# Kernel tuning notes

Measured on AMD Instinct MI355X. Metric: run time of the kernel, lower is better.

Reference implementation:

```python
import jax, jax.numpy as jnp
import numpy as np
from jax import lax

N_SEEDS = 16
N_SAMPS = 32
IN_C = 3
HID = [32, 64, 64]
K = 3
H = W = 64
EPS = 1e-5


def _uniform(key, shape, bound):
    return jax.random.uniform(key, shape, jnp.float32, -bound, bound)


def setup_inputs() -> dict:
    key = jax.random.key(0)
    keys = jax.random.split(key, 32)
    inp = {"x": jax.random.normal(keys[0], (N_SEEDS, N_SAMPS, IN_C, H, W), jnp.float32)}
    c_in = IN_C
    ki = 1
    for li, c_out in enumerate(HID, start=1):
        fan_in = c_in * K * K
        # kaiming_uniform with a=sqrt(5): gain=sqrt(2/(1+5))=sqrt(1/3); bound=sqrt(3)*gain/sqrt(fan)=1/sqrt(fan)
        wb = 1.0 / np.sqrt(fan_in)
        inp[f"w{li}"] = _uniform(keys[ki], (N_SEEDS * c_out, c_in, K, K), wb); ki += 1
        inp[f"b{li}"] = _uniform(keys[ki], (N_SEEDS * c_out,), wb); ki += 1
        inp[f"g{li}"] = jnp.ones((N_SEEDS * c_out,), jnp.float32)
        inp[f"be{li}"] = jnp.zeros((N_SEEDS * c_out,), jnp.float32)
        c_in = c_out
    return inp


def _layer(h, w, b, g, be):
    # grouped conv: groups = N_SEEDS, OIHW weights, NCHW data, stride 1, pad 1
    h = lax.conv_general_dilated(
        h, w, window_strides=(1, 1), padding=((1, 1), (1, 1)),
        feature_group_count=N_SEEDS,
        dimension_numbers=("NCHW", "OIHW", "NCHW"))
    h = h + b[None, :, None, None]
    # BatchNorm2d, training mode: batch statistics over (N, H, W), biased variance
    mean = jnp.mean(h, axis=(0, 2, 3))
    var = jnp.var(h, axis=(0, 2, 3))
    h = (h - mean[None, :, None, None]) * (g / jnp.sqrt(var + EPS))[None, :, None, None] + be[None, :, None, None]
    return jax.nn.relu(h)


def reference(x, w1, b1, g1, be1, w2, b2, g2, be2, w3, b3, g3, be3):
    S, N, C, Hh, Ww = x.shape  # (n_seeds, n_samps, C, H, W)
    h = jnp.swapaxes(x, 0, 1).reshape(N, S * C, Hh, Ww)
    h = _layer(h, w1, b1, g1, be1)
    h = _layer(h, w2, b2, g2, be2)
    h = _layer(h, w3, b3, g3, be3)
    c_out = HID[-1]
    h = h.reshape(N, S, c_out, Hh, Ww)
    return jnp.swapaxes(h, 0, 1)  # (n_seeds, n_samps, C_out, H, W)
```

## Files before the change

kernel.cpp:

```cpp
#include <hip/hip_runtime.h>
#include <cstddef>
#include <cstdint>

typedef __attribute__((ext_vector_type(8))) _Float16 half8;
typedef __attribute__((ext_vector_type(4))) float f32x4;
typedef _Float16 half_t;

#define NS 16
#define NN 32

static const size_t OFF_H1P = 0;
static const size_t OFF_H2P = 138412032ull;
static const size_t OFF_ZR1 = OFF_H2P + 276824064ull;
static const size_t OFF_ZR2 = OFF_ZR1 + 67584ull;
static const size_t OFF_WT1 = OFF_ZR2 + 135168ull;
static const size_t OFF_WT2 = OFF_WT1 + 55296ull;
static const size_t OFF_WT3 = OFF_WT2 + 589824ull;
static const size_t OFF_SUMS = OFF_WT3 + 1179648ull;
static const size_t OFF_PRM = OFF_SUMS + 20480ull;
static const size_t OFF_TH  = OFF_PRM + 30720ull;

static __device__ __forceinline__ half8 sr8(half8 v, half8 t) {
    half8 r = v + t;
    half8 z = {};
#if defined(__has_builtin) && __has_builtin(__builtin_elementwise_max)
    return __builtin_elementwise_max(r, z);
#else
#pragma unroll
    for (int j = 0; j < 8; ++j) r[j] = r[j] > (_Float16)0 ? r[j] : (_Float16)0;
    return r;
#endif
}

__global__ __launch_bounds__(256) void transform1_k(
    const float* __restrict__ w1, float* __restrict__ wt1)
{
    int idx = blockIdx.x * 256 + threadIdx.x;
    if (idx >= 13824) return;
    int o = idx & 31, tap = (idx >> 5) % 9, ic = (idx / 288) % 3, s = idx / 864;
    wt1[idx] = w1[((s * 32 + o) * 3 + ic) * 9 + tap];
}

__global__ __launch_bounds__(256) void wtrans2_k(
    const float* __restrict__ w2, const float* __restrict__ a1, half_t* __restrict__ wt2)
{
    int idx = blockIdx.x * 256 + threadIdx.x;
    if (idx >= 294912) return;
    int ic = idx & 31, oc = (idx >> 5) & 63, tap = (idx >> 11) % 9, s = idx / 18432;
    wt2[idx] = (half_t)(w2[((s * 64 + oc) * 32 + ic) * 9 + tap] * a1[s * 32 + ic]);
}

__global__ __launch_bounds__(256) void wtrans3_k(
    const float* __restrict__ w3, const float* __restrict__ a2, half_t* __restrict__ wt3)
{
    int idx = blockIdx.x * 256 + threadIdx.x;
    if (idx >= 589824) return;
    int ic = idx & 63, oc = (idx >> 6) & 63, tap = (idx >> 12) % 9, s = idx / 36864;
    wt3[idx] = (half_t)(w3[((s * 64 + oc) * 64 + ic) * 9 + tap] * a2[s * 64 + ic]);
}

__global__ __launch_bounds__(256) void conv1_k(
    const float* __restrict__ x, const float* __restrict__ wt1,
    const float* __restrict__ b1, half_t* __restrict__ h1p,
    float* __restrict__ sums1)
{
    __shared__ float smem[8512];
    float* xt = smem;
    float* bounce = smem;
    float* statsl = smem + 8448;
    const int tile = blockIdx.x, s = blockIdx.y, n = blockIdx.z;
    const int tx = tile & 3, ty = tile >> 2, tid = threadIdx.x;

    for (int i = tid; i < 972; i += 256) {
        int ic = i / 324, rem = i - ic * 324;
        int py = rem / 18, px = rem - py * 18;
        int gy = ty * 16 + py - 1, gx = tx * 16 + px - 1;
        float v = 0.f;
        if ((unsigned)gy < 64u && (unsigned)gx < 64u)
            v = x[(size_t)(((s * NN + n) * 3 + ic) * 64 + gy) * 64 + gx];
        xt[i] = v;
    }
    if (tid < 64) statsl[tid] = 0.f;
    __syncthreads();

    const int px = tid & 15, py = tid >> 4;
    float acc[32];
#pragma unroll
    for (int o = 0; o < 32; ++o) acc[o] = 0.f;
#pragma unroll
    for (int ic = 0; ic < 3; ++ic)
#pragma unroll
        for (int ky = 0; ky < 3; ++ky)
#pragma unroll
            for (int kx = 0; kx < 3; ++kx) {
                float v = xt[ic * 324 + (py + ky) * 18 + px + kx];
                const float* wp = wt1 + ((s * 3 + ic) * 9 + ky * 3 + kx) * 32;
#pragma unroll
                for (int o = 0; o < 32; ++o) acc[o] = fmaf(wp[o], v, acc[o]);
            }
    const float* bp = b1 + s * 32;
#pragma unroll
    for (int o = 0; o < 32; ++o) acc[o] += bp[o];

    const int gy1 = ty * 16 + py, gxp = tx * 16 + px + 1;
    half8* dst = (half8*)(h1p + (size_t)(n * NS + s) * 135168 + (size_t)(gy1 * 66 + gxp) * 32);
#pragma unroll
    for (int k = 0; k < 4; ++k) {
        half8 v8;
#pragma unroll
        for (int j = 0; j < 8; ++j) v8[j] = (half_t)acc[k * 8 + j];
        dst[k] = v8;
    }
    __syncthreads();
#pragma unroll
    for (int o = 0; o < 32; ++o) bounce[tid * 33 + o] = acc[o];
    __syncthreads();
    {
        const int oc = tid & 31, grp = tid >> 5;
        float s1 = 0.f, s2 = 0.f;
#pragma unroll 4
        for (int j = 0; j < 32; ++j) {
            float v = bounce[(grp * 32 + j) * 33 + oc];
            s1 += v; s2 += v * v;
        }
        atomicAdd(&statsl[oc * 2], s1);
        atomicAdd(&statsl[oc * 2 + 1], s2);
    }
    __syncthreads();
    if (tid < 64)
        atomicAdd(&sums1[(s * 32 + (tid >> 1)) * 2 + (tid & 1)], statsl[tid]);
}

__global__ void bnparam_k(const float* __restrict__ sums, const float* __restrict__ g,
                          const float* __restrict__ be, float* __restrict__ a,
                          float* __restrict__ b, float* __restrict__ t,
                          half_t* __restrict__ th, int C)
{
    int ch = blockIdx.x * 256 + threadIdx.x;
    if (ch >= C) return;
    const float inv = 1.f / 131072.f;
    float mean = sums[ch * 2] * inv;
    float var = sums[ch * 2 + 1] * inv - mean * mean;
    float sc = g[ch] * rsqrtf(var + 1e-5f);
    a[ch] = sc;
    float bb = be[ch] - mean * sc;
    b[ch] = bb;
    float tt = bb / sc;
    t[ch] = tt;
    th[ch] = (half_t)tt;
}

__global__ __launch_bounds__(256) void padfill_k(
    half_t* __restrict__ img, half_t* __restrict__ zrow, const float* __restrict__ t,
    int C, int c8shift, long imgstride, int rowstride, long tot_cols, long tot)
{
    long idx = (long)blockIdx.x * 256 + threadIdx.x;
    if (idx >= tot) return;
    const int nc8m = (1 << c8shift) - 1;
    if (idx < tot_cols) {
        int c8 = (int)idx & nc8m; long r = idx >> c8shift;
        int side = (int)r & 1; r >>= 1;
        int y = (int)r & 63; r >>= 6;
        int si = (int)(r & 15); int ni = (int)(r >> 4);
        half8 q;
#pragma unroll
        for (int j = 0; j < 8; ++j) q[j] = (half_t)(-(t[si * C + c8 * 8 + j] + 1.0f));
        *(half8*)(img + (long)(ni * NS + si) * imgstride + (long)y * rowstride +
                  (side ? 65 : 0) * C + c8 * 8) = q;
    } else {
        long r2 = idx - tot_cols;
        int c8 = (int)r2 & nc8m; r2 >>= c8shift;
        int xx = (int)(r2 % 66); int si = (int)(r2 / 66);
        half8 q;
#pragma unroll
        for (int j = 0; j < 8; ++j) q[j] = (half_t)(-(t[si * C + c8 * 8 + j] + 1.0f));
        *(half8*)(zrow + ((long)(si * 66 + xx)) * C + c8 * 8) = q;
    }
}

__device__ __forceinline__ void loadB2(half8 bf[4], const half_t* wb, int tap, int l15, int g) {
#pragma unroll
    for (int nt = 0; nt < 4; ++nt)
        bf[nt] = *(const half8*)(wb + (tap * 64 + nt * 16 + l15) * 32 + g * 8);
}

__device__ __forceinline__ void comp2(f32x4 acc[4][4], const half8 bf[4], const char* smem,
                                      int tap, int wv, int l15, int g) {
    const int ky = tap / 3, kx = tap - ky * 3;
#pragma unroll
    for (int mt = 0; mt < 4; ++mt) {
        int p = (wv * 4 + mt + ky) * 18 + l15 + kx;
        half8 av = *(const half8*)(smem + p * 80 + g * 16);
#pragma unroll
        for (int nt = 0; nt < 4; ++nt)
            acc[mt][nt] = __builtin_amdgcn_mfma_f32_16x16x32_f16(av, bf[nt], acc[mt][nt], 0, 0, 0);
    }
}

__global__ __launch_bounds__(256, 3) void conv2_k(
    const half_t* __restrict__ h1p, const half_t* __restrict__ zr1,
    const half_t* __restrict__ wt2, const float* __restrict__ b2,
    const half_t* __restrict__ th1, half_t* __restrict__ h2p,
    float* __restrict__ sums2)
{
    __shared__ __align__(16) char smem[37376];
    float* statsl = (float*)(smem + 36864);
    const int tile = blockIdx.x, s = blockIdx.y, n = blockIdx.z;
    const int tx = tile & 3, ty = tile >> 2, tid = threadIdx.x;
    const int l = tid & 63, wv = tid >> 6, l15 = l & 15, g = l >> 4;
    if (tid < 128) statsl[tid] = 0.f;

    const half_t* wb = wt2 + (size_t)s * 18432;
    half8 bfa[4], bfb[4];
    loadB2(bfa, wb, 0, l15, g);

    const half_t* img = h1p + (size_t)(n * NS + s) * 135168;
    const half_t* zrow = zr1 + s * 2112;
    const int j = tid & 3;
    const half8 tshj = *(const half8*)(th1 + s * 32 + j * 8);
    for (int i = tid; i < 1296; i += 256) {
        int p = i >> 2;
        int py = p / 18, pxx = p - py * 18;
        int gy = ty * 16 + py - 1;
        const half_t* rp = ((unsigned)gy < 64u) ? (img + (size_t)gy * 2112) : zrow;
        half8 v = sr8(*(const half8*)(rp + (tx * 16 + pxx) * 32 + j * 8), tshj);
        *(half8*)(smem + p * 80 + j * 16) = v;
    }
    __syncthreads();

    f32x4 acc[4][4];
#pragma unroll
    for (int mt = 0; mt < 4; ++mt)
#pragma unroll
        for (int nt = 0; nt < 4; ++nt) acc[mt][nt] = (f32x4){0.f, 0.f, 0.f, 0.f};

#pragma unroll
    for (int tap = 0; tap < 9; ++tap) {
        if (tap & 1) {
            if (tap < 8) loadB2(bfa, wb, tap + 1, l15, g);
            comp2(acc, bfb, smem, tap, wv, l15, g);
        } else {
            if (tap < 8) loadB2(bfb, wb, tap + 1, l15, g);
            comp2(acc, bfa, smem, tap, wv, l15, g);
        }
    }

    float s1a[4], s2a[4];
#pragma unroll
    for (int nt = 0; nt < 4; ++nt) {
        float bias = b2[s * 64 + nt * 16 + l15];
        float s1 = 0.f, s2 = 0.f;
#pragma unroll
        for (int mt = 0; mt < 4; ++mt)
#pragma unroll
            for (int r = 0; r < 4; ++r) {
                float v = acc[mt][nt][r] + bias;
                acc[mt][nt][r] = v;
                s1 += v; s2 += v * v;
            }
        s1 += __shfl_xor(s1, 16); s1 += __shfl_xor(s1, 32);
        s2 += __shfl_xor(s2, 16); s2 += __shfl_xor(s2, 32);
        s1a[nt] = s1; s2a[nt] = s2;
    }
    if (l < 16) {
#pragma unroll
        for (int nt = 0; nt < 4; ++nt) {
            atomicAdd(&statsl[(nt * 16 + l15) * 2], s1a[nt]);
            atomicAdd(&statsl[(nt * 16 + l15) * 2 + 1], s2a[nt]);
        }
    }
    __syncthreads();

    half_t* obuf = (half_t*)smem;
#pragma unroll
    for (int mt = 0; mt < 4; ++mt)
#pragma unroll
        for (int nt = 0; nt < 4; ++nt)
#pragma unroll
            for (int r = 0; r < 4; ++r)
                obuf[((wv * 4 + mt) * 16 + g * 4 + r) * 72 + nt * 16 + l15] = (half_t)acc[mt][nt][r];
    __syncthreads();

    half_t* img2 = h2p + (size_t)(n * NS + s) * 270336;
    for (int i = tid; i < 2048; i += 256) {
        int p = i >> 3, cc = i & 7;
        int y = ty * 16 + (p >> 4), xp = tx * 16 + (p & 15) + 1;
        *(half8*)(img2 + (size_t)y * 4224 + xp * 64 + cc * 8) = *(const half8*)(obuf + p * 72 + cc * 8);
    }
    if (tid < 128)
        atomicAdd(&sums2[(s * 64 + (tid >> 1)) * 2 + (tid & 1)], statsl[tid]);
}

__device__ __forceinline__ void loadB3(half8 bf[4][2], const half_t* wb, int tap, int l15, int g) {
#pragma unroll
    for (int nt = 0; nt < 4; ++nt) {
        const half_t* r = wb + (tap * 64 + nt * 16 + l15) * 64 + g * 8;
        bf[nt][0] = *(const half8*)(r);
        bf[nt][1] = *(const half8*)(r + 32);
    }
}

__device__ __forceinline__ void comp3(f32x4 acc[4][4], const half8 bf[4][2], const char* smem,
                                      int tap, int wv, int l15, int g) {
    const int ky = tap / 3, kx = tap - ky * 3;
#pragma unroll
    for (int mt = 0; mt < 4; ++mt) {
        int p = (wv * 4 + mt + ky) * 18 + l15 + kx;
        int base = p * 128, sw = (p & 7) << 4;
        half8 a0 = *(const half8*)(smem + base + ((g * 16) ^ sw));
        half8 a1 = *(const half8*)(smem + base + ((64 + g * 16) ^ sw));
#pragma unroll
        for (int nt = 0; nt < 4; ++nt) {
            acc[mt][nt] = __builtin_amdgcn_mfma_f32_16x16x32_f16(a0, bf[nt][0], acc[mt][nt], 0, 0, 0);
            acc[mt][nt] = __builtin_amdgcn_mfma_f32_16x16x32_f16(a1, bf[nt][1], acc[mt][nt], 0, 0, 0);
        }
    }
}

__global__ __launch_bounds__(256, 3) void conv3_k(
    const half_t* __restrict__ h2p, const half_t* __restrict__ zr2,
    const half_t* __restrict__ wt3, const float* __restrict__ b3,
    const half_t* __restrict__ th2, float* __restrict__ out,
    float* __restrict__ sums3)
{
    __shared__ __align__(16) char smem[41984];
    float* statsl = (float*)(smem + 41472);
    const int tile = blockIdx.x, s = blockIdx.y, n = blockIdx.z;
    const int tx = tile & 3, ty = tile >> 2, tid = threadIdx.x;
    const int l = tid & 63, wv = tid >> 6, l15 = l & 15, g = l >> 4;
    if (tid < 128) statsl[tid] = 0.f;

    const half_t* wb = wt3 + (size_t)s * 36864;
    half8 bfa[4][2], bfb[4][2];
    loadB3(bfa, wb, 0, l15, g);

    const half_t* img = h2p + (size_t)(n * NS + s) * 270336;
    const half_t* zrow = zr2 + s * 4224;
    const int j = tid & 7;
    const half8 tshj = *(const half8*)(th2 + s * 64 + j * 8);
    for (int i = tid; i < 2592; i += 256) {
        int p = i >> 3;
        int py = p / 18, pxx = p - py * 18;
        int gy = ty * 16 + py - 1;
        const half_t* rp = ((unsigned)gy < 64u) ? (img + (size_t)gy * 4224) : zrow;
        half8 v = sr8(*(const half8*)(rp + (tx * 16 + pxx) * 64 + j * 8), tshj);
        *(half8*)(smem + p * 128 + ((j * 16) ^ ((p & 7) << 4))) = v;
    }
    __syncthreads();

    f32x4 acc[4][4];
#pragma unroll
    for (int mt = 0; mt < 4; ++mt)
#pragma unroll
        for (int nt = 0; nt < 4; ++nt) acc[mt][nt] = (f32x4){0.f, 0.f, 0.f, 0.f};

#pragma unroll
    for (int tap = 0; tap < 9; ++tap) {
        if (tap & 1) {
            if (tap < 8) loadB3(bfa, wb, tap + 1, l15, g);
            comp3(acc, bfb, smem, tap, wv, l15, g);
        } else {
            if (tap < 8) loadB3(bfb, wb, tap + 1, l15, g);
            comp3(acc, bfa, smem, tap, wv, l15, g);
        }
    }

    float s1a[4], s2a[4];
#pragma unroll
    for (int nt = 0; nt < 4; ++nt) {
        float bias = b3[s * 64 + nt * 16 + l15];
        float s1 = 0.f, s2 = 0.f;
#pragma unroll
        for (int mt = 0; mt < 4; ++mt)
#pragma unroll
            for (int r = 0; r < 4; ++r) {
                float v = acc[mt][nt][r] + bias;
                acc[mt][nt][r] = v;
                s1 += v; s2 += v * v;
            }
        s1 += __shfl_xor(s1, 16); s1 += __shfl_xor(s1, 32);
        s2 += __shfl_xor(s2, 16); s2 += __shfl_xor(s2, 32);
        s1a[nt] = s1; s2a[nt] = s2;
    }
    if (l < 16) {
#pragma unroll
        for (int nt = 0; nt < 4; ++nt) {
            atomicAdd(&statsl[(nt * 16 + l15) * 2], s1a[nt]);
            atomicAdd(&statsl[(nt * 16 + l15) * 2 + 1], s2a[nt]);
        }
    }

#pragma unroll
    for (int mt = 0; mt < 4; ++mt) {
        int gy = ty * 16 + wv * 4 + mt;
#pragma unroll
        for (int nt = 0; nt < 4; ++nt) {
            int c = nt * 16 + l15;
            *(f32x4*)(out + ((size_t)((s * NN + n) * 64 + c) * 64 + gy) * 64 + tx * 16 + g * 4) = acc[mt][nt];
        }
    }
    __syncthreads();
    if (tid < 128)
        atomicAdd(&sums3[(s * 64 + (tid >> 1)) * 2 + (tid & 1)], statsl[tid]);
}

__global__ __launch_bounds__(256) void final_k(float* __restrict__ out,
                                               const float* __restrict__ a3,
                                               const float* __restrict__ b3p)
{
    size_t i = ((size_t)blockIdx.x * 256 + threadIdx.x) * 4;
    int ch = (int)((i >> 12) & 63) + (int)(i >> 23) * 64;
    float sc = a3[ch], sh = b3p[ch];
    f32x4 v = *(f32x4*)(out + i);
#pragma unroll
    for (int r = 0; r < 4; ++r) v[r] = fmaxf(fmaf(sc, v[r], sh), 0.f);
    *(f32x4*)(out + i) = v;
}

extern "C" void kernel_launch(void* const* d_in, const int* in_sizes, int n_in,
                              void* d_out, int out_size, void* d_ws, size_t ws_size,
                              hipStream_t stream)
{
    const float* x   = (const float*)d_in[0];
    const float* w1  = (const float*)d_in[1];
    const float* b1  = (const float*)d_in[2];
    const float* g1  = (const float*)d_in[3];
    const float* be1 = (const float*)d_in[4];
    const float* w2  = (const float*)d_in[5];
    const float* b2  = (const float*)d_in[6];
    const float* g2  = (const float*)d_in[7];
    const float* be2 = (const float*)d_in[8];
    const float* w3  = (const float*)d_in[9];
    const float* b3  = (const float*)d_in[10];
    const float* g3  = (const float*)d_in[11];
    const float* be3 = (const float*)d_in[12];

    char* ws = (char*)d_ws;
    half_t* h1p = (half_t*)(ws + OFF_H1P);
    half_t* h2p = (half_t*)(ws + OFF_H2P);
    half_t* zr1 = (half_t*)(ws + OFF_ZR1);
    half_t* zr2 = (half_t*)(ws + OFF_ZR2);
    float*  wt1 = (float*)(ws + OFF_WT1);
    half_t* wt2 = (half_t*)(ws + OFF_WT2);
    half_t* wt3 = (half_t*)(ws + OFF_WT3);
    float*  sums = (float*)(ws + OFF_SUMS);
    float *s1v = sums, *s2v = sums + 1024, *s3v = sums + 3072;
    float*  prm = (float*)(ws + OFF_PRM);
    float *a1 = prm,        *b1p = prm + 512,  *t1 = prm + 1024;
    float *a2 = prm + 1536, *b2p = prm + 2560, *t2 = prm + 3584;
    float *a3 = prm + 4608, *b3p = prm + 5632, *t3 = prm + 6656;
    half_t* th = (half_t*)(ws + OFF_TH);
    half_t *th1 = th, *th2 = th + 512, *th3 = th + 1536;
    float* out = (float*)d_out;

    hipMemsetAsync(ws + OFF_SUMS, 0, 20480, stream);
    transform1_k<<<54, 256, 0, stream>>>(w1, wt1);
    dim3 grid(16, 16, 32);
    conv1_k<<<grid, 256, 0, stream>>>(x, wt1, b1, h1p, s1v);
    bnparam_k<<<2, 256, 0, stream>>>(s1v, g1, be1, a1, b1p, t1, th1, 512);
    padfill_k<<<1041, 256, 0, stream>>>(h1p, zr1, t1, 32, 2, 135168L, 2112, 262144L, 266368L);
    wtrans2_k<<<1152, 256, 0, stream>>>(w2, a1, wt2);
    conv2_k<<<grid, 256, 0, stream>>>(h1p, zr1, wt2, b2, th1, h2p, s2v);
    bnparam_k<<<4, 256, 0, stream>>>(s2v, g2, be2, a2, b2p, t2, th2, 1024);
    padfill_k<<<2081, 256, 0, stream>>>(h2p, zr2, t2, 64, 3, 270336L, 4224, 524288L, 532736L);
    wtrans3_k<<<2304, 256, 0, stream>>>(w3, a2, wt3);
    conv3_k<<<grid, 256, 0, stream>>>(h2p, zr2, wt3, b3, th2, out, s3v);
    bnparam_k<<<4, 256, 0, stream>>>(s3v, g3, be3, a3, b3p, t3, th3, 1024);
    final_k<<<131072, 256, 0, stream>>>(out, a3, b3p);
}
```

Measured before the change: 1.002 ms.

## Retile conv3 into full-width 4-row strips with 512 threads split over output channels

The third conv kernel now gives each block a 4-row by 64-column strip instead of a 16x16 tile, and runs 8 waves, each covering one row and half of the output channels. The wider tile makes the fp32 output writes contiguous along full image rows and cuts per-wave accumulator registers in half. The cost is a larger input halo per block (6x66 versus 18x18 pixels) and more shared memory, with occupancy now set by the 512-thread launch bounds.

```diff
diff --git a/kernel.cpp b/kernel.cpp
--- a/kernel.cpp
+++ b/kernel.cpp
@@ -291,84 +291,86 @@
         atomicAdd(&sums2[(s * 64 + (tid >> 1)) * 2 + (tid & 1)], statsl[tid]);
 }
 
-__device__ __forceinline__ void loadB3(half8 bf[4][2], const half_t* wb, int tap, int l15, int g) {
-#pragma unroll
-    for (int nt = 0; nt < 4; ++nt) {
-        const half_t* r = wb + (tap * 64 + nt * 16 + l15) * 64 + g * 8;
+__device__ __forceinline__ void loadB3(half8 bf[2][2], const half_t* wb, int tap,
+                                       int och, int l15, int g) {
+#pragma unroll
+    for (int nt = 0; nt < 2; ++nt) {
+        const half_t* r = wb + (tap * 64 + och * 32 + nt * 16 + l15) * 64 + g * 8;
         bf[nt][0] = *(const half8*)(r);
         bf[nt][1] = *(const half8*)(r + 32);
     }
 }
 
-__device__ __forceinline__ void comp3(f32x4 acc[4][4], const half8 bf[4][2], const char* smem,
-                                      int tap, int wv, int l15, int g) {
+__device__ __forceinline__ void comp3(f32x4 acc[4][2], const half8 bf[2][2], const char* smem,
+                                      int tap, int wy, int l15, int g) {
     const int ky = tap / 3, kx = tap - ky * 3;
 #pragma unroll
     for (int mt = 0; mt < 4; ++mt) {
-        int p = (wv * 4 + mt + ky) * 18 + l15 + kx;
+        int p = (wy + ky) * 66 + mt * 16 + l15 + kx;
         int base = p * 128, sw = (p & 7) << 4;
         half8 a0 = *(const half8*)(smem + base + ((g * 16) ^ sw));
         half8 a1 = *(const half8*)(smem + base + ((64 + g * 16) ^ sw));
 #pragma unroll
-        for (int nt = 0; nt < 4; ++nt) {
+        for (int nt = 0; nt < 2; ++nt) {
             acc[mt][nt] = __builtin_amdgcn_mfma_f32_16x16x32_f16(a0, bf[nt][0], acc[mt][nt], 0, 0, 0);
             acc[mt][nt] = __builtin_amdgcn_mfma_f32_16x16x32_f16(a1, bf[nt][1], acc[mt][nt], 0, 0, 0);
         }
     }
 }
 
-__global__ __launch_bounds__(256, 3) void conv3_k(
+__global__ __launch_bounds__(512, 4) void conv3_k(
     const half_t* __restrict__ h2p, const half_t* __restrict__ zr2,
     const half_t* __restrict__ wt3, const float* __restrict__ b3,
     const half_t* __restrict__ th2, float* __restrict__ out,
     float* __restrict__ sums3)
 {
-    __shared__ __align__(16) char smem[41984];
-    float* statsl = (float*)(smem + 41472);
-    const int tile = blockIdx.x, s = blockIdx.y, n = blockIdx.z;
-    const int tx = tile & 3, ty = tile >> 2, tid = threadIdx.x;
-    const int l = tid & 63, wv = tid >> 6, l15 = l & 15, g = l >> 4;
+    __shared__ __align__(16) char smem[51200];
+    float* statsl = (float*)(smem + 50688);
+    const int ty = blockIdx.x, s = blockIdx.y, n = blockIdx.z;
+    const int tid = threadIdx.x;
+    const int l = tid & 63, w = tid >> 6, l15 = l & 15, g = l >> 4;
+    const int wy = w & 3, och = w >> 2;
     if (tid < 128) statsl[tid] = 0.f;
 
     const half_t* wb = wt3 + (size_t)s * 36864;
-    half8 bfa[4][2], bfb[4][2];
-    loadB3(bfa, wb, 0, l15, g);
+    half8 bfa[2][2], bfb[2][2];
+    loadB3(bfa, wb, 0, och, l15, g);
 
     const half_t* img = h2p + (size_t)(n * NS + s) * 270336;
     const half_t* zrow = zr2 + s * 4224;
     const int j = tid & 7;
     const half8 tshj = *(const half8*)(th2 + s * 64 + j * 8);
-    for (int i = tid; i < 2592; i += 256) {
+    for (int i = tid; i < 3168; i += 512) {
         int p = i >> 3;
-        int py = p / 18, pxx = p - py * 18;
-        int gy = ty * 16 + py - 1;
+        int row = p / 66, col = p - row * 66;
+        int gy = ty * 4 + row - 1;
         const half_t* rp = ((unsigned)gy < 64u) ? (img + (size_t)gy * 4224) : zrow;
-        half8 v = sr8(*(const half8*)(rp + (tx * 16 + pxx) * 64 + j * 8), tshj);
+        half8 v = sr8(*(const half8*)(rp + col * 64 + j * 8), tshj);
         *(half8*)(smem + p * 128 + ((j * 16) ^ ((p & 7) << 4))) = v;
     }
     __syncthreads();
 
-    f32x4 acc[4][4];
+    f32x4 acc[4][2];
 #pragma unroll
     for (int mt = 0; mt < 4; ++mt)
 #pragma unroll
-        for (int nt = 0; nt < 4; ++nt) acc[mt][nt] = (f32x4){0.f, 0.f, 0.f, 0.f};
+        for (int nt = 0; nt < 2; ++nt) acc[mt][nt] = (f32x4){0.f, 0.f, 0.f, 0.f};
 
 #pragma unroll
     for (int tap = 0; tap < 9; ++tap) {
         if (tap & 1) {
-            if (tap < 8) loadB3(bfa, wb, tap + 1, l15, g);
-            comp3(acc, bfb, smem, tap, wv, l15, g);
+            if (tap < 8) loadB3(bfa, wb, tap + 1, och, l15, g);
+            comp3(acc, bfb, smem, tap, wy, l15, g);
         } else {
-            if (tap < 8) loadB3(bfb, wb, tap + 1, l15, g);
-            comp3(acc, bfa, smem, tap, wv, l15, g);
-        }
-    }
-
-    float s1a[4], s2a[4];
-#pragma unroll
-    for (int nt = 0; nt < 4; ++nt) {
-        float bias = b3[s * 64 + nt * 16 + l15];
+            if (tap < 8) loadB3(bfb, wb, tap + 1, och, l15, g);
+            comp3(acc, bfa, smem, tap, wy, l15, g);
+        }
+    }
+
+    float s1a[2], s2a[2];
+#pragma unroll
+    for (int nt = 0; nt < 2; ++nt) {
+        float bias = b3[s * 64 + och * 32 + nt * 16 + l15];
         float s1 = 0.f, s2 = 0.f;
 #pragma unroll
         for (int mt = 0; mt < 4; ++mt)
@@ -384,21 +386,20 @@
     }
     if (l < 16) {
 #pragma unroll
-        for (int nt = 0; nt < 4; ++nt) {
-            atomicAdd(&statsl[(nt * 16 + l15) * 2], s1a[nt]);
-            atomicAdd(&statsl[(nt * 16 + l15) * 2 + 1], s2a[nt]);
-        }
-    }
-
-#pragma unroll
-    for (int mt = 0; mt < 4; ++mt) {
-        int gy = ty * 16 + wv * 4 + mt;
-#pragma unroll
-        for (int nt = 0; nt < 4; ++nt) {
-            int c = nt * 16 + l15;
-            *(f32x4*)(out + ((size_t)((s * NN + n) * 64 + c) * 64 + gy) * 64 + tx * 16 + g * 4) = acc[mt][nt];
-        }
-    }
+        for (int nt = 0; nt < 2; ++nt) {
+            atomicAdd(&statsl[(och * 32 + nt * 16 + l15) * 2], s1a[nt]);
+            atomicAdd(&statsl[(och * 32 + nt * 16 + l15) * 2 + 1], s2a[nt]);
+        }
+    }
+
+    const int gy = ty * 4 + wy;
+#pragma unroll
+    for (int mt = 0; mt < 4; ++mt)
+#pragma unroll
+        for (int nt = 0; nt < 2; ++nt) {
+            int c = och * 32 + nt * 16 + l15;
+            *(f32x4*)(out + ((size_t)((s * NN + n) * 64 + c) * 64 + gy) * 64 + mt * 16 + g * 4) = acc[mt][nt];
+        }
     __syncthreads();
     if (tid < 128)
         atomicAdd(&sums3[(s * 64 + (tid >> 1)) * 2 + (tid & 1)], statsl[tid]);
@@ -464,7 +465,8 @@
     bnparam_k<<<4, 256, 0, stream>>>(s2v, g2, be2, a2, b2p, t2, th2, 1024);
     padfill_k<<<2081, 256, 0, stream>>>(h2p, zr2, t2, 64, 3, 270336L, 4224, 524288L, 532736L);
     wtrans3_k<<<2304, 256, 0, stream>>>(w3, a2, wt3);
-    conv3_k<<<grid, 256, 0, stream>>>(h2p, zr2, wt3, b3, th2, out, s3v);
+    dim3 grid3(16, 16, 32);
+    conv3_k<<<grid3, 512, 0, stream>>>(h2p, zr2, wt3, b3, th2, out, s3v);
     bnparam_k<<<4, 256, 0, stream>>>(s3v, g3, be3, a3, b3p, t3, th3, 1024);
     final_k<<<131072, 256, 0, stream>>>(out, a3, b3p);
 }
```

Result: faster. 877.0 us (-12.4%).
